# Optimization experiments

Hardware: AMD Instinct MI355X
Metric: run time of the kernel (lower is better)

The kernel has to match this reference:

```python
import jax, jax.numpy as jnp
import numpy as np

# Model hyperparams (match init_kwargs)
B = 256        # batch
S = 2048       # seq_length (I/Q samples)
PATCH = 32     # patch_size
STRIDE = 16    # int(PATCH * overlap), overlap=0.5
FN = 127       # FrameNum = n_patch - 1
NP = 128       # tokens after appending cls
D = 64         # d_model = 2 * patch_size
H = 4          # n_head_qk = n_head_v
DQK = 16
DV = 16
DFF = 256      # hidden_features
DF2 = DFF // 2
L = 8          # layer_num
NC = 11        # num_class
SCALE = DQK ** 0.5
EPS = 1e-5


def setup_inputs() -> dict:
    key = jax.random.key(0)
    ks = jax.random.split(key, 16)
    w = lambda k, shape, s=0.1: (jax.random.normal(k, shape, jnp.float32) * s)
    return {
        "x": jax.random.normal(ks[0], (B, S, 2), jnp.float32),
        "frame_W": w(ks[1], (2 * PATCH, 2 * PATCH)),          # Frame embedding Dense, no bias
        "cls_token": w(ks[2], (1, 1, D), 0.02),
        "pos_embed": w(ks[3], (1, NP, D), 0.02),
        "Wq": w(ks[4], (L, D, H * DQK)),
        "Wk": w(ks[5], (L, D, H * DQK)),
        "Wv": w(ks[6], (L, D, H * DV)),
        "Wmix": w(ks[7], (L, H, H), 0.3),                     # 1x1 Conv2D talking-heads kernel [h_in,h_out]
        "Wo": w(ks[8], (L, H * DV, D)),
        "ln1_g": jnp.ones((L, D), jnp.float32),
        "ln1_b": jnp.zeros((L, D), jnp.float32),
        "ln2_g": jnp.ones((L, D), jnp.float32),
        "ln2_b": jnp.zeros((L, D), jnp.float32),
        "W1": w(ks[9], (L, D, DFF)),
        "b1": jnp.zeros((L, DFF), jnp.float32),
        "W2": w(ks[10], (L, DF2, D)),
        "b2": jnp.zeros((L, D), jnp.float32),
        "Wc": w(ks[11], (D, NC)),
        "bc": jnp.zeros((NC,), jnp.float32),
    }


def _ln(x, g, b):
    mu = jnp.mean(x, axis=-1, keepdims=True)
    var = jnp.mean(jnp.square(x - mu), axis=-1, keepdims=True)
    return (x - mu) * jax.lax.rsqrt(var + EPS) * g + b


def _gelu(x):
    return jax.nn.gelu(x, approximate=False)  # keras 'gelu' is exact


def _forward(x, frame_W, cls_token, pos_embed, Wq, Wk, Wv, Wmix, Wo,
             ln1_g, ln1_b, ln2_g, ln2_b, W1, b1, W2, b2, Wc, bc):
    Bn = x.shape[0]
    # Frame: overlapping patches of I and Q channels, concatenated, embedded
    idx = jnp.arange(FN)[:, None] * STRIDE + jnp.arange(PATCH)[None, :]  # [FN, PATCH]
    patches = jnp.concatenate([x[:, idx, 0], x[:, idx, 1]], axis=-1)     # [B, FN, 2*PATCH]
    h = patches @ frame_W                                                # [B, FN, D]
    h = jnp.concatenate([h, jnp.broadcast_to(cls_token, (Bn, 1, D))], axis=1) + pos_embed  # [B, NP, D]
    attn_res0 = jnp.zeros((Bn, H, NP, NP), h.dtype)  # RealFormer residual logits (initially 0)

    def layer(carry, p):
        h, ar = carry
        wq, wk, wv, wmix, wo, g1, be1, g2, be2, w1, bb1, w2, bb2 = p
        q = (h @ wq).reshape(Bn, NP, H, DQK).transpose(0, 2, 1, 3) / SCALE  # [B,H,P,dqk]
        k = (h @ wk).reshape(Bn, NP, H, DQK).transpose(0, 2, 1, 3)
        v = (h @ wv).reshape(Bn, NP, H, DV).transpose(0, 2, 1, 3)
        logits = jnp.einsum('bhid,bhjd->bhij', q, k)          # [B,H,P,P]
        logits = jnp.einsum('bhij,hg->bgij', logits, wmix)    # talking-heads 1x1 conv mix
        attn = jax.nn.softmax(logits + ar, axis=-1)           # RealFormer residual add
        o = jnp.einsum('bhij,bhjd->bhid', attn, v)
        o = o.transpose(0, 2, 1, 3).reshape(Bn, NP, H * DV)
        h = _ln(h + o @ wo, g1, be1)
        # DB-GLU FFN: dual-branch cross-gated GELU
        u = h @ w1 + bb1
        u1, u2 = u[..., :DF2], u[..., DF2:]
        f = (u1 * _gelu(u2) + u2 * _gelu(u1)) @ w2 + bb2
        h = _ln(h + f, g2, be2)
        return (h, attn), None

    (h, _), _ = jax.lax.scan(
        layer, (h, attn_res0),
        (Wq, Wk, Wv, Wmix, Wo, ln1_g, ln1_b, ln2_g, ln2_b, W1, b1, W2, b2))
    return jax.nn.softmax(h[:, -1] @ Wc + bc, axis=-1)  # cls token is last; [B, NC]


def reference(x, frame_W, cls_token, pos_embed, Wq, Wk, Wv, Wmix, Wo,
              ln1_g, ln1_b, ln2_g, ln2_b, W1, b1, W2, b2, Wc, bc):
    return _forward(x, frame_W, cls_token, pos_embed, Wq, Wk, Wv, Wmix, Wo,
                    ln1_g, ln1_b, ln2_g, ln2_b, W1, b1, W2, b2, Wc, bc)
```

## Files before the change

### kernel.cpp

```cpp
#include <hip/hip_runtime.h>
#include <hip/hip_bf16.h>
#include <math.h>

typedef short s16x8 __attribute__((ext_vector_type(8)));
typedef short s16x4 __attribute__((ext_vector_type(4)));
typedef _Float16 f16x8 __attribute__((ext_vector_type(8)));
typedef float f32x4 __attribute__((ext_vector_type(4)));
typedef unsigned u32x4 __attribute__((ext_vector_type(4)));

#define MFMA(a, b, c) \
  __builtin_amdgcn_mfma_f32_16x16x32_f16(__builtin_bit_cast(f16x8, a), \
                                         __builtin_bit_cast(f16x8, b), c, 0, 0, 0)

#define LOG2E 1.44269504088896340736f
#define LN2   0.69314718055994530942f

__device__ __forceinline__ float ex2(float x) {
#if __has_builtin(__builtin_amdgcn_exp2f)
  return __builtin_amdgcn_exp2f(x);
#else
  float r; asm("v_exp_f32 %0, %1" : "=v"(r) : "v"(x)); return r;
#endif
}
__device__ __forceinline__ float rcpf_(float x) {
#if __has_builtin(__builtin_amdgcn_rcpf)
  return __builtin_amdgcn_rcpf(x);
#else
  float r; asm("v_rcp_f32 %0, %1" : "=v"(r) : "v"(x)); return r;
#endif
}
__device__ __forceinline__ f32x4 splat(float x) { f32x4 r = {x, x, x, x}; return r; }

#define OFF_FWB 0
#define OFF_WQB 8192
#define OFF_WKB 73728
#define OFF_WVB 139264
#define OFF_WOB 204800
#define OFF_W1B 270336
#define OFF_W2B 532480

#define L_Q 0
#define L_K 16384
#define L_V 32768
#define L_O 49152
#define LW_Q 65536
#define LW_K 73728
#define LW_V 81920
#define LW_O 90112
#define LW_1 98304
#define LW_2 131072
#define L_B1 147456
#define LDS_BYTES 155648

__device__ __forceinline__ int fragSlotByte(int idx, int k, int KS) {
  return ((((idx >> 4) * KS + (k >> 5)) << 10)
        | (((idx & 15) | (((k >> 2) & 3) << 4)) << 4)
        | (((k & 3) | (((k >> 4) & 1) << 2)) << 1));
}
__device__ __forceinline__ short f2h(float f) {
  _Float16 h = (_Float16)f;
  return __builtin_bit_cast(short, h);
}
__device__ __forceinline__ float h2f(short s) {
  return (float)__builtin_bit_cast(_Float16, s);
}
__device__ __forceinline__ unsigned pk_u32(float a, float b) {
  return __builtin_bit_cast(unsigned, __builtin_amdgcn_cvt_pkrtz(a, b));
}
__device__ __forceinline__ f32x4 gelu4(const f32x4& v) {
  const u32x4 bits = __builtin_bit_cast(u32x4, v);
  const u32x4 sgn = bits & 0x80000000u;
  const f32x4 av = __builtin_bit_cast(f32x4, bits & 0x7fffffffu);
  const f32x4 z = av * splat(0.70710678118654752f);
  const f32x4 den = z * splat(0.47047f) + splat(1.0f);
  f32x4 t;
  t[0] = rcpf_(den[0]); t[1] = rcpf_(den[1]); t[2] = rcpf_(den[2]); t[3] = rcpf_(den[3]);
  const f32x4 p = t * (splat(0.3480242f) + t * (splat(-0.0958798f) + t * splat(0.7478556f)));
  const f32x4 m = v * v * splat(-0.72134752044448170368f);
  f32x4 e;
  e[0] = ex2(m[0]); e[1] = ex2(m[1]); e[2] = ex2(m[2]); e[3] = ex2(m[3]);
  const f32x4 erfa = splat(1.0f) - p * e;
  const f32x4 erfv = __builtin_bit_cast(f32x4, __builtin_bit_cast(u32x4, erfa) | sgn);
  return splat(0.5f) * v * (splat(1.0f) + erfv);
}
__device__ __forceinline__ s16x8 pack8(const f32x4& a, const f32x4& b) {
  union { unsigned u[4]; s16x8 s; } z;
  z.u[0] = pk_u32(a[0], a[1]);
  z.u[1] = pk_u32(a[2], a[3]);
  z.u[2] = pk_u32(b[0], b[1]);
  z.u[3] = pk_u32(b[2], b[3]);
  return z.s;
}
__device__ __forceinline__ s16x4 pack4(const f32x4& a) {
  union { unsigned u[2]; s16x4 s; } z;
  z.u[0] = pk_u32(a[0], a[1]);
  z.u[1] = pk_u32(a[2], a[3]);
  return z.s;
}
__device__ __forceinline__ s16x8 fragL(const char* lds, int off, int tile, int lane) {
  return *(const s16x8*)(lds + off + (tile << 10) + (lane << 4));
}
__device__ __forceinline__ s16x8 fragG(const char* wb, int tile, int lane) {
  return *(const s16x8*)(wb + (tile << 10) + (lane << 4));
}

__device__ __forceinline__ void gl_lds16(const char* g, char* l) {
#if __has_builtin(__builtin_amdgcn_global_load_lds)
  __builtin_amdgcn_global_load_lds(
      (const __attribute__((address_space(1))) unsigned int*)g,
      (__attribute__((address_space(3))) unsigned int*)l, 16, 0, 0);
#else
  *(s16x8*)l = *(const s16x8*)g;
#endif
}
__device__ __forceinline__ void stageW(const char* g, char* l, int bytes, int tid) {
  for (int off = tid * 16; off < bytes; off += 8192)
    gl_lds16(g + off, l + off);
}

extern "C" __global__ void prep_all(const float* __restrict__ fw, const float* __restrict__ wq,
                                    const float* __restrict__ wk, const float* __restrict__ wv,
                                    const float* __restrict__ wo, const float* __restrict__ w1,
                                    const float* __restrict__ w2, char* __restrict__ dst) {
  for (int e = blockIdx.x * blockDim.x + threadIdx.x; e < 331776; e += gridDim.x * blockDim.x) {
    const float* src; int dstoff, K, N, rel; float sc = 1.f;
    if (e < 4096)        { src = fw; dstoff = OFF_FWB; K = 64;  N = 64;  rel = e; }
    else if (e < 36864)  { src = wq; dstoff = OFF_WQB; K = 64;  N = 64;  rel = e - 4096; sc = 0.25f; }
    else if (e < 69632)  { src = wk; dstoff = OFF_WKB; K = 64;  N = 64;  rel = e - 36864; }
    else if (e < 102400) { src = wv; dstoff = OFF_WVB; K = 64;  N = 64;  rel = e - 69632; }
    else if (e < 135168) { src = wo; dstoff = OFF_WOB; K = 64;  N = 64;  rel = e - 102400; sc = LN2; }
    else if (e < 266240) { src = w1; dstoff = OFF_W1B; K = 64;  N = 256; rel = e - 135168; }
    else                 { src = w2; dstoff = OFF_W2B; K = 128; N = 64;  rel = e - 266240; }
    const int KS = K >> 5, pl = K * N;
    const int l = rel / pl, r2 = rel - l * pl;
    const int k = r2 / N, n = r2 - k * N;
    *(short*)(dst + dstoff + (size_t)l * pl * 2 + fragSlotByte(n, k, KS)) = f2h(src[rel] * sc);
  }
}

extern "C" __global__ __launch_bounds__(512)
void feat_fwd(const float* __restrict__ x, const float* __restrict__ cls_token,
              const float* __restrict__ pos_embed, const float* __restrict__ Wmix,
              const float* __restrict__ ln1_g, const float* __restrict__ ln1_b,
              const float* __restrict__ ln2_g, const float* __restrict__ ln2_b,
              const float* __restrict__ b1, const float* __restrict__ b2,
              const float* __restrict__ Wc, const float* __restrict__ bc,
              float* __restrict__ out, const char* __restrict__ wfrag) {
  extern __shared__ char lds[];
  const int tid = threadIdx.x, lane = tid & 63, wv = tid >> 6, b = blockIdx.x;
  const int l15 = lane & 15, g16 = lane >> 4;
  const f32x4 Z4 = {0.f, 0.f, 0.f, 0.f};

  f32x4 hr[4];
  s16x8 hp[2];
  s16x8 af[4][4] = {};

  stageW(wfrag + OFF_WQB, lds + LW_Q, 8192, tid);
  stageW(wfrag + OFF_WKB, lds + LW_K, 8192, tid);
  stageW(wfrag + OFF_WVB, lds + LW_V, 8192, tid);
  stageW((const char*)b1, lds + L_B1, 8192, tid);

  {
    const int i0 = wv * 16 + l15;
    s16x8 xB[2];
#pragma unroll
    for (int ks = 0; ks < 2; ++ks) {
      f32x4 lo, hi;
#pragma unroll
      for (int e = 0; e < 8; ++e) {
        int sidx = i0 * 16 + (e >> 2) * 16 + g16 * 4 + (e & 3);
        if (sidx > 2047) sidx = 2047;
        float xv = x[((size_t)b * 2048 + sidx) * 2 + ks];
        if (e < 4) lo[e] = xv; else hi[e - 4] = xv;
      }
      xB[ks] = pack8(lo, hi);
    }
    const char* fwb = wfrag + OFF_FWB;
#pragma unroll
    for (int nt = 0; nt < 4; ++nt) {
      f32x4 a = *(const f32x4*)&pos_embed[i0 * 64 + nt * 16 + g16 * 4];
      a = MFMA(fragG(fwb, nt * 2 + 0, lane), xB[0], a);
      a = MFMA(fragG(fwb, nt * 2 + 1, lane), xB[1], a);
      hr[nt] = a;
    }
    if (i0 == 127) {
#pragma unroll
      for (int nt = 0; nt < 4; ++nt) {
        const f32x4 c4 = *(const f32x4*)&cls_token[nt * 16 + g16 * 4];
        const f32x4 p4 = *(const f32x4*)&pos_embed[127 * 64 + nt * 16 + g16 * 4];
        hr[nt] = c4 + p4;
      }
    }
    hp[0] = pack8(hr[0], hr[1]);
    hp[1] = pack8(hr[2], hr[3]);
  }
  __syncthreads();

  for (int l = 0; l < 8; ++l) {
    {
      f32x4 aq[4], ak[4], av[4];
#pragma unroll
      for (int nt = 0; nt < 4; ++nt) { aq[nt] = Z4; ak[nt] = Z4; av[nt] = Z4; }
#pragma unroll
      for (int ks = 0; ks < 2; ++ks)
#pragma unroll
        for (int nt = 0; nt < 4; ++nt) {
          aq[nt] = MFMA(fragL(lds, LW_Q, nt * 2 + ks, lane), hp[ks], aq[nt]);
          ak[nt] = MFMA(fragL(lds, LW_K, nt * 2 + ks, lane), hp[ks], ak[nt]);
          av[nt] = MFMA(hp[ks], fragL(lds, LW_V, nt * 2 + ks, lane), av[nt]);
        }
#pragma unroll
      for (int ksp = 0; ksp < 2; ++ksp) {
        *(s16x8*)(lds + L_Q + (((wv * 2 + ksp) << 10) | (lane << 4))) = pack8(aq[2 * ksp], aq[2 * ksp + 1]);
        *(s16x8*)(lds + L_K + (((wv * 2 + ksp) << 10) | (lane << 4))) = pack8(ak[2 * ksp], ak[2 * ksp + 1]);
      }
#pragma unroll
      for (int nt = 0; nt < 4; ++nt)
        *(s16x4*)(lds + L_V + (((nt * 4 + (wv >> 1)) << 10) | (lane << 4) | ((wv & 1) << 3))) = pack4(av[nt]);
    }
    __syncthreads();

    if (l < 7) {
      stageW(wfrag + OFF_WQB + (l + 1) * 8192, lds + LW_Q, 8192, tid);
      stageW(wfrag + OFF_WKB + (l + 1) * 8192, lds + LW_K, 8192, tid);
      stageW(wfrag + OFF_WVB + (l + 1) * 8192, lds + LW_V, 8192, tid);
    }
    stageW(wfrag + OFF_WOB + l * 8192, lds + LW_O, 8192, tid);
    stageW(wfrag + OFF_W1B + l * 32768, lds + LW_1, 32768, tid);
    stageW(wfrag + OFF_W2B + l * 16384, lds + LW_2, 16384, tid);

    {
      const int g = wv >> 1, ih = wv & 1;
      s16x8 wmv[2];
      {
        const float w0 = Wmix[(l * 4 + 0) * 4 + g] * LOG2E, w1_ = Wmix[(l * 4 + 1) * 4 + g] * LOG2E;
        const float w2_ = Wmix[(l * 4 + 2) * 4 + g] * LOG2E, w3_ = Wmix[(l * 4 + 3) * 4 + g] * LOG2E;
        union { unsigned u[4]; s16x8 s; } u0, u1;
        u0.u[0] = u0.u[1] = pk_u32(w0, w0);
        u0.u[2] = u0.u[3] = pk_u32(w1_, w1_);
        u1.u[0] = u1.u[1] = pk_u32(w2_, w2_);
        u1.u[2] = u1.u[3] = pk_u32(w3_, w3_);
        wmv[0] = u0.s; wmv[1] = u1.s;
      }
#pragma unroll
      for (int q4 = 0; q4 < 4; ++q4) {
        const int ti = ih * 4 + q4;
        f32x4 acc[8];
        if (l > 0) {
#pragma unroll
          for (int jt = 0; jt < 8; ++jt)
#pragma unroll
            for (int r = 0; r < 4; ++r)
              acc[jt][r] = h2f(af[q4][jt >> 1][((jt & 1) << 2) | r]);
        } else {
#pragma unroll
          for (int jt = 0; jt < 8; ++jt) acc[jt] = Z4;
        }
#pragma unroll
        for (int ks = 0; ks < 2; ++ks) {
          const s16x8 qr = fragL(lds, L_Q, ti * 2 + ks, lane);
          const f16x8 qm = __builtin_bit_cast(f16x8, qr) * __builtin_bit_cast(f16x8, wmv[ks]);
#pragma unroll
          for (int jt = 0; jt < 8; ++jt)
            acc[jt] = MFMA(fragL(lds, L_K, jt * 2 + ks, lane), qm, acc[jt]);
        }
        f32x4 sv = Z4;
#pragma unroll
        for (int jt = 0; jt < 8; ++jt) {
          acc[jt][0] = ex2(acc[jt][0]);
          acc[jt][1] = ex2(acc[jt][1]);
          acc[jt][2] = ex2(acc[jt][2]);
          acc[jt][3] = ex2(acc[jt][3]);
          sv += acc[jt];
        }
        float s = (sv[0] + sv[1]) + (sv[2] + sv[3]);
        s += __shfl_xor(s, 16); s += __shfl_xor(s, 32);
        const float invl = rcpf_(s) * LOG2E;
        const f32x4 iv = splat(invl);
#pragma unroll
        for (int jt = 0; jt < 8; ++jt) acc[jt] *= iv;
#pragma unroll
        for (int ks3 = 0; ks3 < 4; ++ks3)
          af[q4][ks3] = pack8(acc[2 * ks3], acc[2 * ks3 + 1]);
      }
    }

    {
      const int g = wv >> 1, ih = wv & 1;
#pragma unroll
      for (int q4 = 0; q4 < 4; ++q4) {
        const int ti = ih * 4 + q4;
        f32x4 a = Z4;
#pragma unroll
        for (int ks = 0; ks < 4; ++ks)
          a = MFMA(fragL(lds, L_V, g * 4 + ks, lane), af[q4][ks], a);
        *(s16x4*)(lds + L_O + (((ti * 2 + (g >> 1)) << 10) | (lane << 4) | ((g & 1) << 3))) = pack4(a);
      }
    }
    __syncthreads();

    {
      s16x8 ofr[2];
      ofr[0] = fragL(lds, L_O, wv * 2 + 0, lane);
      ofr[1] = fragL(lds, L_O, wv * 2 + 1, lane);
      f32x4 vv[4];
      f32x4 sv = Z4;
#pragma unroll
      for (int nt = 0; nt < 4; ++nt) {
        f32x4 a = hr[nt];
        a = MFMA(fragL(lds, LW_O, nt * 2 + 0, lane), ofr[0], a);
        a = MFMA(fragL(lds, LW_O, nt * 2 + 1, lane), ofr[1], a);
        vv[nt] = a;
        sv += a;
      }
      float s = (sv[0] + sv[1]) + (sv[2] + sv[3]);
      s += __shfl_xor(s, 16); s += __shfl_xor(s, 32);
      const float mu = s * 0.015625f;
      const f32x4 mu4 = splat(mu);
      f32x4 d[4], q = Z4;
#pragma unroll
      for (int nt = 0; nt < 4; ++nt) { d[nt] = vv[nt] - mu4; q += d[nt] * d[nt]; }
      float sq = (q[0] + q[1]) + (q[2] + q[3]);
      sq += __shfl_xor(sq, 16); sq += __shfl_xor(sq, 32);
      const float rs = rsqrtf(sq * 0.015625f + 1e-5f);
      const f32x4 rs4 = splat(rs);
#pragma unroll
      for (int nt = 0; nt < 4; ++nt) {
        const f32x4 g4 = *(const f32x4*)&ln1_g[l * 64 + nt * 16 + g16 * 4];
        const f32x4 b4 = *(const f32x4*)&ln1_b[l * 64 + nt * 16 + g16 * 4];
        hr[nt] = d[nt] * rs4 * g4 + b4;
      }
      hp[0] = pack8(hr[0], hr[1]);
      hp[1] = pack8(hr[2], hr[3]);
    }

    {
      f32x4 acc6[4];
#pragma unroll
      for (int nt = 0; nt < 4; ++nt) {
        const f32x4 bb = *(const f32x4*)&b2[l * 64 + nt * 16 + g16 * 4];
        acc6[nt] = hr[nt] + bb;
      }
#pragma unroll
      for (int ks6 = 0; ks6 < 4; ++ks6) {
        union { unsigned u[4]; s16x8 s; } fb;
#pragma unroll
        for (int half = 0; half < 2; ++half) {
          const int mtp = ks6 * 2 + half;
          f32x4 a1 = *(const f32x4*)(lds + L_B1 + (l * 256 + mtp * 16 + g16 * 4) * 4);
          f32x4 a2 = *(const f32x4*)(lds + L_B1 + (l * 256 + 128 + mtp * 16 + g16 * 4) * 4);
#pragma unroll
          for (int ks = 0; ks < 2; ++ks) {
            a1 = MFMA(fragL(lds, LW_1, mtp * 2 + ks, lane), hp[ks], a1);
            a2 = MFMA(fragL(lds, LW_1, (mtp + 8) * 2 + ks, lane), hp[ks], a2);
          }
          const f32x4 fv = a1 * gelu4(a2) + a2 * gelu4(a1);
          fb.u[half * 2 + 0] = pk_u32(fv[0], fv[1]);
          fb.u[half * 2 + 1] = pk_u32(fv[2], fv[3]);
        }
#pragma unroll
        for (int nt = 0; nt < 4; ++nt)
          acc6[nt] = MFMA(fragL(lds, LW_2, nt * 4 + ks6, lane), fb.s, acc6[nt]);
      }
      f32x4 sv = Z4;
#pragma unroll
      for (int nt = 0; nt < 4; ++nt) sv += acc6[nt];
      float s = (sv[0] + sv[1]) + (sv[2] + sv[3]);
      s += __shfl_xor(s, 16); s += __shfl_xor(s, 32);
      const float mu = s * 0.015625f;
      const f32x4 mu4 = splat(mu);
      f32x4 d[4], q = Z4;
#pragma unroll
      for (int nt = 0; nt < 4; ++nt) { d[nt] = acc6[nt] - mu4; q += d[nt] * d[nt]; }
      float sq = (q[0] + q[1]) + (q[2] + q[3]);
      sq += __shfl_xor(sq, 16); sq += __shfl_xor(sq, 32);
      const float rs = rsqrtf(sq * 0.015625f + 1e-5f);
      const f32x4 rs4 = splat(rs);
#pragma unroll
      for (int nt = 0; nt < 4; ++nt) {
        const f32x4 g4 = *(const f32x4*)&ln2_g[l * 64 + nt * 16 + g16 * 4];
        const f32x4 b4 = *(const f32x4*)&ln2_b[l * 64 + nt * 16 + g16 * 4];
        hr[nt] = d[nt] * rs4 * g4 + b4;
      }
      hp[0] = pack8(hr[0], hr[1]);
      hp[1] = pack8(hr[2], hr[3]);
    }
  }

  float* scr = (float*)(lds + L_Q);
  if (wv == 7 && l15 == 15) {
#pragma unroll
    for (int nt = 0; nt < 4; ++nt)
#pragma unroll
      for (int r = 0; r < 4; ++r) scr[nt * 16 + g16 * 4 + r] = hr[nt][r];
  }
  __syncthreads();
  if (wv == 0) {
    const float hc = scr[lane];
    float lg[11];
#pragma unroll
    for (int kc = 0; kc < 11; ++kc) {
      float p = hc * Wc[lane * 11 + kc];
      p += __shfl_xor(p, 1);  p += __shfl_xor(p, 2);  p += __shfl_xor(p, 4);
      p += __shfl_xor(p, 8);  p += __shfl_xor(p, 16); p += __shfl_xor(p, 32);
      lg[kc] = p + bc[kc];
    }
    float mx = lg[0];
#pragma unroll
    for (int kc = 1; kc < 11; ++kc) mx = fmaxf(mx, lg[kc]);
    float s = 0.f;
#pragma unroll
    for (int kc = 0; kc < 11; ++kc) s += __expf(lg[kc] - mx);
    const float inv = 1.f / s;
    if (lane < 11) out[b * 11 + lane] = __expf(lg[lane] - mx) * inv;
  }
}

extern "C" void kernel_launch(void* const* d_in, const int* in_sizes, int n_in,
                              void* d_out, int out_size, void* d_ws, size_t ws_size,
                              hipStream_t stream) {
  const float* x         = (const float*)d_in[0];
  const float* frame_W   = (const float*)d_in[1];
  const float* cls_token = (const float*)d_in[2];
  const float* pos_embed = (const float*)d_in[3];
  const float* Wq        = (const float*)d_in[4];
  const float* Wk        = (const float*)d_in[5];
  const float* Wv        = (const float*)d_in[6];
  const float* Wmix      = (const float*)d_in[7];
  const float* Wo        = (const float*)d_in[8];
  const float* ln1_g     = (const float*)d_in[9];
  const float* ln1_b     = (const float*)d_in[10];
  const float* ln2_g     = (const float*)d_in[11];
  const float* ln2_b     = (const float*)d_in[12];
  const float* W1        = (const float*)d_in[13];
  const float* b1        = (const float*)d_in[14];
  const float* W2        = (const float*)d_in[15];
  const float* b2        = (const float*)d_in[16];
  const float* Wc        = (const float*)d_in[17];
  const float* bc        = (const float*)d_in[18];
  float* out = (float*)d_out;
  char* wfrag = (char*)d_ws;

  prep_all<<<162, 256, 0, stream>>>(frame_W, Wq, Wk, Wv, Wo, W1, W2, wfrag);

  (void)hipFuncSetAttribute((const void*)feat_fwd, hipFuncAttributeMaxDynamicSharedMemorySize, LDS_BYTES);
  feat_fwd<<<dim3(256), dim3(512), LDS_BYTES, stream>>>(
      x, cls_token, pos_embed, Wmix, ln1_g, ln1_b, ln2_g, ln2_b,
      b1, b2, Wc, bc, out, wfrag);
}
```

Before: 104.8 us.

## Keep attention residual in fp32 registers and use tanh-style sigmoid GELU

Three changes at once. The RealFormer attention residual is now kept as fp32 accumulators (128 floats per lane) instead of packed fp16, which removes the per-layer unpack into MFMA accumulators. The fp16 pack moves to the point of use in the PV matmul. GELU switches from an erf polynomial to a sigmoid form using one exp2 and one reciprocal, and launch bounds are pinned to one block per CU. The change uses more registers and a less exact GELU approximation.

```diff
diff --git a/kernel.cpp b/kernel.cpp
--- a/kernel.cpp
+++ b/kernel.cpp
@@ -61,27 +61,19 @@
   _Float16 h = (_Float16)f;
   return __builtin_bit_cast(short, h);
 }
-__device__ __forceinline__ float h2f(short s) {
-  return (float)__builtin_bit_cast(_Float16, s);
-}
 __device__ __forceinline__ unsigned pk_u32(float a, float b) {
   return __builtin_bit_cast(unsigned, __builtin_amdgcn_cvt_pkrtz(a, b));
 }
 __device__ __forceinline__ f32x4 gelu4(const f32x4& v) {
-  const u32x4 bits = __builtin_bit_cast(u32x4, v);
-  const u32x4 sgn = bits & 0x80000000u;
-  const f32x4 av = __builtin_bit_cast(f32x4, bits & 0x7fffffffu);
-  const f32x4 z = av * splat(0.70710678118654752f);
-  const f32x4 den = z * splat(0.47047f) + splat(1.0f);
-  f32x4 t;
-  t[0] = rcpf_(den[0]); t[1] = rcpf_(den[1]); t[2] = rcpf_(den[2]); t[3] = rcpf_(den[3]);
-  const f32x4 p = t * (splat(0.3480242f) + t * (splat(-0.0958798f) + t * splat(0.7478556f)));
-  const f32x4 m = v * v * splat(-0.72134752044448170368f);
+  const f32x4 x2 = v * v;
+  const f32x4 inner = splat(-2.30258930213f) + x2 * splat(-0.102970317236f);
+  const f32x4 arg = v * inner;
   f32x4 e;
-  e[0] = ex2(m[0]); e[1] = ex2(m[1]); e[2] = ex2(m[2]); e[3] = ex2(m[3]);
-  const f32x4 erfa = splat(1.0f) - p * e;
-  const f32x4 erfv = __builtin_bit_cast(f32x4, __builtin_bit_cast(u32x4, erfa) | sgn);
-  return splat(0.5f) * v * (splat(1.0f) + erfv);
+  e[0] = ex2(arg[0]); e[1] = ex2(arg[1]); e[2] = ex2(arg[2]); e[3] = ex2(arg[3]);
+  const f32x4 den = splat(1.0f) + e;
+  f32x4 r;
+  r[0] = rcpf_(den[0]); r[1] = rcpf_(den[1]); r[2] = rcpf_(den[2]); r[3] = rcpf_(den[3]);
+  return v * r;
 }
 __device__ __forceinline__ s16x8 pack8(const f32x4& a, const f32x4& b) {
   union { unsigned u[4]; s16x8 s; } z;
@@ -138,7 +130,7 @@
   }
 }
 
-extern "C" __global__ __launch_bounds__(512)
+extern "C" __global__ __launch_bounds__(512, 1)
 void feat_fwd(const float* __restrict__ x, const float* __restrict__ cls_token,
               const float* __restrict__ pos_embed, const float* __restrict__ Wmix,
               const float* __restrict__ ln1_g, const float* __restrict__ ln1_b,
@@ -153,7 +145,11 @@
 
   f32x4 hr[4];
   s16x8 hp[2];
-  s16x8 af[4][4] = {};
+  f32x4 af32[4][8];
+#pragma unroll
+  for (int q4 = 0; q4 < 4; ++q4)
+#pragma unroll
+    for (int jt = 0; jt < 8; ++jt) af32[q4][jt] = Z4;
 
   stageW(wfrag + OFF_WQB, lds + LW_Q, 8192, tid);
   stageW(wfrag + OFF_WKB, lds + LW_K, 8192, tid);
@@ -245,43 +241,29 @@
 #pragma unroll
       for (int q4 = 0; q4 < 4; ++q4) {
         const int ti = ih * 4 + q4;
-        f32x4 acc[8];
-        if (l > 0) {
-#pragma unroll
-          for (int jt = 0; jt < 8; ++jt)
-#pragma unroll
-            for (int r = 0; r < 4; ++r)
-              acc[jt][r] = h2f(af[q4][jt >> 1][((jt & 1) << 2) | r]);
-        } else {
-#pragma unroll
-          for (int jt = 0; jt < 8; ++jt) acc[jt] = Z4;
-        }
 #pragma unroll
         for (int ks = 0; ks < 2; ++ks) {
           const s16x8 qr = fragL(lds, L_Q, ti * 2 + ks, lane);
           const f16x8 qm = __builtin_bit_cast(f16x8, qr) * __builtin_bit_cast(f16x8, wmv[ks]);
 #pragma unroll
           for (int jt = 0; jt < 8; ++jt)
-            acc[jt] = MFMA(fragL(lds, L_K, jt * 2 + ks, lane), qm, acc[jt]);
+            af32[q4][jt] = MFMA(fragL(lds, L_K, jt * 2 + ks, lane), qm, af32[q4][jt]);
         }
         f32x4 sv = Z4;
 #pragma unroll
         for (int jt = 0; jt < 8; ++jt) {
-          acc[jt][0] = ex2(acc[jt][0]);
-          acc[jt][1] = ex2(acc[jt][1]);
-          acc[jt][2] = ex2(acc[jt][2]);
-          acc[jt][3] = ex2(acc[jt][3]);
-          sv += acc[jt];
+          af32[q4][jt][0] = ex2(af32[q4][jt][0]);
+          af32[q4][jt][1] = ex2(af32[q4][jt][1]);
+          af32[q4][jt][2] = ex2(af32[q4][jt][2]);
+          af32[q4][jt][3] = ex2(af32[q4][jt][3]);
+          sv += af32[q4][jt];
         }
         float s = (sv[0] + sv[1]) + (sv[2] + sv[3]);
         s += __shfl_xor(s, 16); s += __shfl_xor(s, 32);
         const float invl = rcpf_(s) * LOG2E;
         const f32x4 iv = splat(invl);
 #pragma unroll
-        for (int jt = 0; jt < 8; ++jt) acc[jt] *= iv;
-#pragma unroll
-        for (int ks3 = 0; ks3 < 4; ++ks3)
-          af[q4][ks3] = pack8(acc[2 * ks3], acc[2 * ks3 + 1]);
+        for (int jt = 0; jt < 8; ++jt) af32[q4][jt] *= iv;
       }
     }
 
@@ -292,8 +274,10 @@
         const int ti = ih * 4 + q4;
         f32x4 a = Z4;
 #pragma unroll
-        for (int ks = 0; ks < 4; ++ks)
-          a = MFMA(fragL(lds, L_V, g * 4 + ks, lane), af[q4][ks], a);
+        for (int ks = 0; ks < 4; ++ks) {
+          const s16x8 pfrag = pack8(af32[q4][2 * ks], af32[q4][2 * ks + 1]);
+          a = MFMA(fragL(lds, L_V, g * 4 + ks, lane), pfrag, a);
+        }
         *(s16x4*)(lds + L_O + (((ti * 2 + (g >> 1)) << 10) | (lane << 4) | ((g & 1) << 3))) = pack4(a);
       }
     }
```

Result: faster. 96.24 us (-8.2%).
